# Performance work log

Hardware: AMD Instinct MI355X
Metric: run time of the kernel (lower is better)

The kernel has to match this reference:

```python
import jax, jax.numpy as jnp
import numpy as np

N, DIN, DOUT, E, K = 65536, 256, 256, 8, 2

def setup_inputs() -> dict:
    key = jax.random.key(0)
    k1, k2, k3, k4 = jax.random.split(key, 4)
    x = jax.random.normal(k1, (N, DIN), dtype=jnp.float32)
    Wr = jax.random.normal(k2, (DIN, E), dtype=jnp.float32) * (DIN ** -0.5)   # router Linear (no bias)
    We = jax.random.normal(k3, (E, DIN, DOUT), dtype=jnp.float32) * (DIN ** -0.5)  # expert Linear weights
    be = jax.random.normal(k4, (E, DOUT), dtype=jnp.float32) * 0.01               # expert Linear biases
    return {"x": x, "Wr": Wr, "We": We, "be": be}

def reference(x, Wr, We, be):
    # router: softmax over experts (eval mode -> no noise)
    probs = jax.nn.softmax(x @ Wr, axis=1)                    # [N, E]
    w, sel = jax.lax.top_k(probs, K)                          # [N, K]
    w = w / jnp.sum(w, axis=1, keepdims=True)                 # renormalize top-k weights
    # dense combine weights: scatter top-k weights back to [N, E]
    combine = jnp.zeros_like(probs).at[jnp.arange(x.shape[0])[:, None], sel].add(w)
    # all-expert outputs, then weighted combine (same math as gather/matmul/index_add loop)
    y_all = jnp.einsum('ni,eio->neo', x, We) + be[None, :, :]  # [N, E, DOUT]
    out = jnp.einsum('neo,ne->no', y_all, combine)             # [N, DOUT]
    return out
```

## Files before the change

kernel.cpp:

```cpp
#include <hip/hip_runtime.h>

#define N_TOK 65536
#define DIN   256
#define DOUT  256
#define NEXP  8
#define NPAIR 28

typedef __bf16 bf16x8 __attribute__((ext_vector_type(8)));
typedef __bf16 bf16x4 __attribute__((ext_vector_type(4)));
typedef float  f32x4  __attribute__((ext_vector_type(4)));

__device__ __forceinline__ void cp16_g2l(const void* g, void* l) {
  auto gp = (const __attribute__((address_space(1))) unsigned int*)(unsigned long long)g;
  auto lp = (__attribute__((address_space(3))) unsigned int*)(unsigned long long)l;
  __builtin_amdgcn_global_load_lds(gp, lp, 16, 0, 0);
}

__global__ __launch_bounds__(256) void prep_kernel(const float* __restrict__ We,
                                                   __bf16* __restrict__ Wt,
                                                   int* __restrict__ cnt) {
  __shared__ float T[64 * 65];
  int bid = blockIdx.x;
  if (bid == 0 && threadIdx.x < NPAIR) cnt[threadIdx.x] = 0;
  int e = bid >> 4;
  int tk = (bid >> 2) & 3, tn = bid & 3;
  int k0 = tk * 64, n0 = tn * 64;
  int tid = threadIdx.x;
  int cr = tid >> 6;
  int cc = tid & 63;
#pragma unroll
  for (int i = 0; i < 16; i++) {
    int k = i * 4 + cr;
    T[cc * 65 + k] = We[(size_t)(e * 256 + k0 + k) * 256 + n0 + cc];
  }
  __syncthreads();
#pragma unroll
  for (int i = 0; i < 16; i++) {
    int n = i * 4 + cr;
    Wt[(size_t)(e * 256 + n0 + n) * 256 + k0 + cc] = (__bf16)T[n * 65 + cc];
  }
}

__global__ __launch_bounds__(256) void router_kernel(const float* __restrict__ x,
                                                     const float* __restrict__ Wr,
                                                     __bf16* __restrict__ xb,
                                                     int* __restrict__ cnt,
                                                     unsigned short* __restrict__ pidx,
                                                     float* __restrict__ pw) {
  __shared__ float X[64 * 64];
  __shared__ float P[64 * 36];
  __shared__ int lcnt[NPAIR];
  __shared__ int gbase[NPAIR];
  int tid = threadIdx.x;
  if (tid < NPAIR) lcnt[tid] = 0;

  const int w = __builtin_amdgcn_readfirstlane(tid >> 6);
  const int t = tid & 63;
  int tokBase = blockIdx.x * 64;

  const int srow = tid >> 4;
  const int so16 = tid & 15;
  const int spo  = so16 ^ (srow & 7);

  float acc[NEXP];
#pragma unroll
  for (int e = 0; e < NEXP; e++) acc[e] = 0.f;

  float4 v[4];
#pragma unroll
  for (int i = 0; i < 4; i++)
    v[i] = *(const float4*)&x[(size_t)(tokBase + srow + 16 * i) * DIN + so16 * 4];

  for (int c = 0; c < 4; c++) {
#pragma unroll
    for (int i = 0; i < 4; i++) {
      int r = srow + 16 * i;
      *(float4*)&X[r * 64 + spo * 4] = v[i];
      bf16x4 bv;
      bv[0] = (__bf16)v[i].x; bv[1] = (__bf16)v[i].y;
      bv[2] = (__bf16)v[i].z; bv[3] = (__bf16)v[i].w;
      *(bf16x4*)&xb[(size_t)(tokBase + r) * DIN + c * 64 + so16 * 4] = bv;
    }
    __syncthreads();
    if (c < 3) {
#pragma unroll
      for (int i = 0; i < 4; i++)
        v[i] = *(const float4*)&x[(size_t)(tokBase + srow + 16 * i) * DIN + (c + 1) * 64 + so16 * 4];
    }
#pragma unroll
    for (int i4 = 0; i4 < 4; i4++) {
      int po = (w * 4 + i4) ^ (t & 7);
      float4 xv = *(const float4*)&X[t * 64 + po * 4];
      const float* w0 = &Wr[(c * 64 + w * 16 + i4 * 4) * NEXP];
#pragma unroll
      for (int e = 0; e < NEXP; e++)
        acc[e] += xv.x * w0[e] + xv.y * w0[NEXP + e] + xv.z * w0[2 * NEXP + e] + xv.w * w0[3 * NEXP + e];
    }
    __syncthreads();
  }

  f32x4 lo, hi;
#pragma unroll
  for (int e = 0; e < 4; e++) { lo[e] = acc[e]; hi[e] = acc[4 + e]; }
  *(f32x4*)&P[t * 36 + w * 8]     = lo;
  *(f32x4*)&P[t * 36 + w * 8 + 4] = hi;
  __syncthreads();
  if (tid >= 64) return;

  int token = tokBase + tid;

  f32x4 pa0 = *(const f32x4*)&P[tid * 36 + 0];
  f32x4 pa1 = *(const f32x4*)&P[tid * 36 + 8];
  f32x4 pa2 = *(const f32x4*)&P[tid * 36 + 16];
  f32x4 pa3 = *(const f32x4*)&P[tid * 36 + 24];
  f32x4 pb0 = *(const f32x4*)&P[tid * 36 + 4];
  f32x4 pb1 = *(const f32x4*)&P[tid * 36 + 12];
  f32x4 pb2 = *(const f32x4*)&P[tid * 36 + 20];
  f32x4 pb3 = *(const f32x4*)&P[tid * 36 + 28];
  f32x4 sA = ((pa0 + pa1) + pa2) + pa3;
  f32x4 sB = ((pb0 + pb1) + pb2) + pb3;
  float lg[NEXP];
#pragma unroll
  for (int e = 0; e < 4; e++) { lg[e] = sA[e]; lg[4 + e] = sB[e]; }

  int best = 0;
#pragma unroll
  for (int e = 1; e < NEXP; e++) if (lg[e] > lg[best]) best = e;
  int sec = (best == 0) ? 1 : 0;
#pragma unroll
  for (int e = 0; e < NEXP; e++)
    if (e != best && e != sec && lg[e] > lg[sec]) sec = e;
  float l3 = -1e30f;
#pragma unroll
  for (int e = 0; e < NEXP; e++)
    if (e != best && e != sec) l3 = fmaxf(l3, lg[e]);

  float diff = lg[sec] - lg[best];
  bool need = (lg[sec] - l3) < 5e-3f;
  if (__any(need)) {
    if (need) {
      const float4* xr = (const float4*)(x + (size_t)token * DIN);
      double d[NEXP];
#pragma unroll
      for (int e = 0; e < NEXP; e++) d[e] = 0.0;
      for (int i4 = 0; i4 < DIN / 4; i4++) {
        float4 vv = xr[i4];
        const float* w0 = &Wr[(i4 * 4) * NEXP];
#pragma unroll
        for (int e = 0; e < NEXP; e++)
          d[e] += (double)vv.x * w0[e] + (double)vv.y * w0[NEXP + e] +
                  (double)vv.z * w0[2 * NEXP + e] + (double)vv.w * w0[3 * NEXP + e];
      }
      best = 0;
#pragma unroll
      for (int e = 1; e < NEXP; e++) if (d[e] > d[best]) best = e;
      sec = (best == 0) ? 1 : 0;
#pragma unroll
      for (int e = 0; e < NEXP; e++)
        if (e != best && e != sec && d[e] > d[sec]) sec = e;
      diff = (float)(d[sec] - d[best]);
    }
  }

  float wb = 1.f / (1.f + expf(diff));
  int a, b2; float wa;
  if (best < sec) { a = best; b2 = sec; wa = wb; }
  else            { a = sec;  b2 = best; wa = 1.f - wb; }
  int p = a * (15 - a) / 2 + (b2 - a - 1);

  int lpos = atomicAdd(&lcnt[p], 1);
  if (tid < NPAIR) gbase[tid] = atomicAdd(&cnt[tid], lcnt[tid]);
  int pos = gbase[p] + lpos;
  pidx[p * N_TOK + pos] = (unsigned short)token;
  pw[p * N_TOK + pos] = wa;
}

__global__ __launch_bounds__(256, 2) void moe_gemm_kernel(const __bf16* __restrict__ xb,
                                                          const __bf16* __restrict__ Wt,
                                                          const float* __restrict__ be,
                                                          const int* __restrict__ cnt,
                                                          const unsigned short* __restrict__ pidx,
                                                          const float* __restrict__ pw,
                                                          float* __restrict__ out) {
  __shared__ __bf16 As[128 * 256];
  __shared__ unsigned short tokL[128];
  __shared__ float wL[128];
  __shared__ int meta[4];

  int tid = threadIdx.x;
  int bid = blockIdx.x;
  int nh = (bid >> 3) & 3;
  int tile = ((bid >> 5) << 3) | (bid & 7);

  if (tid == 0) {
    int s = 0, pp = -1, lt = 0, c = 0;
    for (int q = 0; q < NPAIR; q++) {
      int cq = cnt[q];
      int tq = (cq + 127) >> 7;
      if (tile < s + tq) { pp = q; lt = tile - s; c = cq; break; }
      s += tq;
    }
    meta[0] = pp; meta[1] = lt; meta[2] = c;
  }
  __syncthreads();
  int p = meta[0];
  if (p < 0) return;
  int lt = meta[1], cnt_p = meta[2];

  int a = 0, rem = p;
  while (rem >= 7 - a) { rem -= 7 - a; a++; }
  int b2 = a + 1 + rem;
  int r0 = lt * 128;

  if (tid < 128) {
    int gr = r0 + tid;
    tokL[tid] = (gr < cnt_p) ? pidx[p * N_TOK + gr] : (unsigned short)0;
    wL[tid]   = (gr < cnt_p) ? pw[p * N_TOK + gr] : 0.f;
  }
  __syncthreads();

  {
    const int r_base = tid >> 5;
    const int s8 = (tid & 31) ^ r_base;
#pragma unroll
    for (int i = 0; i < 16; i++) {
      int row = r_base + 8 * i;
      cp16_g2l(xb + (size_t)tokL[row] * DIN + s8 * 8, &As[(size_t)(tid + 256 * i) * 8]);
    }
  }
  __builtin_amdgcn_s_waitcnt(0x0F70);
  __syncthreads();

  const int lane = tid & 63, wid = tid >> 6;
  const int wm = wid & 1, wn = wid >> 1;
  const int c16 = lane & 15, quad = lane >> 4;

  const __bf16* WtA = Wt + ((size_t)a * DOUT + nh * 64) * DIN;
  const __bf16* WtB = Wt + ((size_t)b2 * DOUT + nh * 64) * DIN;

  f32x4 accA[4][2], accB[4][2];
#pragma unroll
  for (int mi = 0; mi < 4; mi++)
#pragma unroll
    for (int ni = 0; ni < 2; ni++)
#pragma unroll
      for (int r = 0; r < 4; r++) { accA[mi][ni][r] = 0.f; accB[mi][ni][r] = 0.f; }

#pragma unroll
  for (int kc = 0; kc < 4; kc++) {
#pragma unroll
    for (int ks = 0; ks < 2; ks++) {
      bf16x8 af[4], ba[2], bb[2];
      int oct = kc * 8 + ks * 4 + quad;
#pragma unroll
      for (int mi = 0; mi < 4; mi++) {
        int row = wm * 64 + mi * 16 + c16;
        af[mi] = *(const bf16x8*)&As[(size_t)(row * 32 + (oct ^ (row & 7))) * 8];
      }
#pragma unroll
      for (int ni = 0; ni < 2; ni++) {
        int col = wn * 32 + ni * 16 + c16;
        int koff = kc * 64 + ks * 32 + quad * 8;
        ba[ni] = *(const bf16x8*)&WtA[(size_t)col * DIN + koff];
        bb[ni] = *(const bf16x8*)&WtB[(size_t)col * DIN + koff];
      }
#pragma unroll
      for (int mi = 0; mi < 4; mi++)
#pragma unroll
        for (int ni = 0; ni < 2; ni++) {
          accA[mi][ni] = __builtin_amdgcn_mfma_f32_16x16x32_bf16(af[mi], ba[ni], accA[mi][ni], 0, 0, 0);
          accB[mi][ni] = __builtin_amdgcn_mfma_f32_16x16x32_bf16(af[mi], bb[ni], accB[mi][ni], 0, 0, 0);
        }
    }
  }

#pragma unroll
  for (int ni = 0; ni < 2; ni++) {
    int gcol = nh * 64 + wn * 32 + ni * 16 + c16;
    float bea = be[a * DOUT + gcol];
    float beb = be[b2 * DOUT + gcol];
#pragma unroll
    for (int mi = 0; mi < 4; mi++) {
#pragma unroll
      for (int r = 0; r < 4; r++) {
        int row = wm * 64 + mi * 16 + quad * 4 + r;
        if (r0 + row < cnt_p) {
          float w = wL[row];
          out[(size_t)tokL[row] * DOUT + gcol] =
              w * (accA[mi][ni][r] + bea) + (1.f - w) * (accB[mi][ni][r] + beb);
        }
      }
    }
  }
}

extern "C" void kernel_launch(void* const* d_in, const int* in_sizes, int n_in,
                              void* d_out, int out_size, void* d_ws, size_t ws_size,
                              hipStream_t stream) {
  const float* x  = (const float*)d_in[0];
  const float* Wr = (const float*)d_in[1];
  const float* We = (const float*)d_in[2];
  const float* be = (const float*)d_in[3];
  float* out = (float*)d_out;

  char* w = (char*)d_ws;
  __bf16* Wt = (__bf16*)w;
  __bf16* xb = (__bf16*)(w + (1u << 20));
  int* cnt = (int*)(w + (33u << 20));
  unsigned short* pidx = (unsigned short*)(w + (33u << 20) + 512);
  float* pw = (float*)(w + (33u << 20) + 512 + (size_t)NPAIR * N_TOK * 2);

  prep_kernel<<<128, 256, 0, stream>>>(We, Wt, cnt);
  router_kernel<<<N_TOK / 64, 256, 0, stream>>>(x, Wr, xb, cnt, pidx, pw);
  moe_gemm_kernel<<<2176, 256, 0, stream>>>(xb, Wt, be, cnt, pidx, pw, out);
}
```

Baseline: 218.6 us.

## Fuse router and dense all-expert GEMM into one per-token-block kernel

Replaces the router kernel (pair bucketing with atomics and scatter) and the gathered pair GEMM with one kernel. Each 64-token block converts x to bf16 in LDS, computes routing weights locally, then runs MFMA over all 8 experts with a weighted accumulate. This removes the bf16 activation round trip, the index/weight buffers, the atomics and a launch. In exchange it does 4x the matrix FLOPs, since the 6 experts with zero combine weight are still computed. The output is staged through LDS for coalesced stores.

```diff
diff --git a/kernel.cpp b/kernel.cpp
--- a/kernel.cpp
+++ b/kernel.cpp
@@ -4,24 +4,14 @@
 #define DIN   256
 #define DOUT  256
 #define NEXP  8
-#define NPAIR 28
 
 typedef __bf16 bf16x8 __attribute__((ext_vector_type(8)));
-typedef __bf16 bf16x4 __attribute__((ext_vector_type(4)));
 typedef float  f32x4  __attribute__((ext_vector_type(4)));
 
-__device__ __forceinline__ void cp16_g2l(const void* g, void* l) {
-  auto gp = (const __attribute__((address_space(1))) unsigned int*)(unsigned long long)g;
-  auto lp = (__attribute__((address_space(3))) unsigned int*)(unsigned long long)l;
-  __builtin_amdgcn_global_load_lds(gp, lp, 16, 0, 0);
-}
-
 __global__ __launch_bounds__(256) void prep_kernel(const float* __restrict__ We,
-                                                   __bf16* __restrict__ Wt,
-                                                   int* __restrict__ cnt) {
+                                                   __bf16* __restrict__ Wt) {
   __shared__ float T[64 * 65];
   int bid = blockIdx.x;
-  if (bid == 0 && threadIdx.x < NPAIR) cnt[threadIdx.x] = 0;
   int e = bid >> 4;
   int tk = (bid >> 2) & 3, tn = bid & 3;
   int k0 = tk * 64, n0 = tn * 64;
@@ -41,255 +31,198 @@
   }
 }
 
-__global__ __launch_bounds__(256) void router_kernel(const float* __restrict__ x,
-                                                     const float* __restrict__ Wr,
-                                                     __bf16* __restrict__ xb,
-                                                     int* __restrict__ cnt,
-                                                     unsigned short* __restrict__ pidx,
-                                                     float* __restrict__ pw) {
-  __shared__ float X[64 * 64];
+__global__ __launch_bounds__(256, 2) void moe_fused_kernel(const float* __restrict__ x,
+                                                           const float* __restrict__ Wr,
+                                                           const __bf16* __restrict__ Wt,
+                                                           const float* __restrict__ be,
+                                                           float* __restrict__ out) {
+  __shared__ __bf16 Xb[64 * 256];
   __shared__ float P[64 * 36];
-  __shared__ int lcnt[NPAIR];
-  __shared__ int gbase[NPAIR];
-  int tid = threadIdx.x;
-  if (tid < NPAIR) lcnt[tid] = 0;
+  __shared__ float C8[NEXP * 64];
+
+  const int tid = threadIdx.x;
+  const int tokBase = blockIdx.x * 64;
+
+  C8[tid] = 0.f;
+  C8[tid + 256] = 0.f;
+
+  {
+    const int srow = tid >> 5;
+    const int so   = tid & 31;
+    const int s8   = so ^ (srow & 7);
+#pragma unroll
+    for (int i = 0; i < 8; i++) {
+      int row = srow + 8 * i;
+      const float* src = &x[(size_t)(tokBase + row) * DIN + s8 * 8];
+      float4 u0 = *(const float4*)src;
+      float4 u1 = *(const float4*)(src + 4);
+      bf16x8 pk;
+      pk[0] = (__bf16)u0.x; pk[1] = (__bf16)u0.y; pk[2] = (__bf16)u0.z; pk[3] = (__bf16)u0.w;
+      pk[4] = (__bf16)u1.x; pk[5] = (__bf16)u1.y; pk[6] = (__bf16)u1.z; pk[7] = (__bf16)u1.w;
+      *(bf16x8*)&Xb[(row * 32 + so) * 8] = pk;
+    }
+  }
 
   const int w = __builtin_amdgcn_readfirstlane(tid >> 6);
   const int t = tid & 63;
-  int tokBase = blockIdx.x * 64;
-
-  const int srow = tid >> 4;
-  const int so16 = tid & 15;
-  const int spo  = so16 ^ (srow & 7);
-
-  float acc[NEXP];
-#pragma unroll
-  for (int e = 0; e < NEXP; e++) acc[e] = 0.f;
-
-  float4 v[4];
-#pragma unroll
-  for (int i = 0; i < 4; i++)
-    v[i] = *(const float4*)&x[(size_t)(tokBase + srow + 16 * i) * DIN + so16 * 4];
-
-  for (int c = 0; c < 4; c++) {
-#pragma unroll
-    for (int i = 0; i < 4; i++) {
-      int r = srow + 16 * i;
-      *(float4*)&X[r * 64 + spo * 4] = v[i];
-      bf16x4 bv;
-      bv[0] = (__bf16)v[i].x; bv[1] = (__bf16)v[i].y;
-      bv[2] = (__bf16)v[i].z; bv[3] = (__bf16)v[i].w;
-      *(bf16x4*)&xb[(size_t)(tokBase + r) * DIN + c * 64 + so16 * 4] = bv;
-    }
+  const int token = tokBase + t;
+  {
+    float a8[NEXP];
+#pragma unroll
+    for (int e = 0; e < NEXP; e++) a8[e] = 0.f;
+#pragma unroll
+    for (int i4 = 0; i4 < 16; i4++) {
+      int k = w * 64 + i4 * 4;
+      float4 xv = *(const float4*)&x[(size_t)token * DIN + k];
+      const float* w0 = &Wr[k * NEXP];
+#pragma unroll
+      for (int e = 0; e < NEXP; e++)
+        a8[e] += xv.x * w0[e] + xv.y * w0[NEXP + e] + xv.z * w0[2 * NEXP + e] + xv.w * w0[3 * NEXP + e];
+    }
+    f32x4 lo, hi;
+#pragma unroll
+    for (int e = 0; e < 4; e++) { lo[e] = a8[e]; hi[e] = a8[4 + e]; }
+    *(f32x4*)&P[t * 36 + w * 8]     = lo;
+    *(f32x4*)&P[t * 36 + w * 8 + 4] = hi;
+  }
+  __syncthreads();
+
+  if (tid < 64) {
+    f32x4 pa0 = *(const f32x4*)&P[tid * 36 + 0];
+    f32x4 pa1 = *(const f32x4*)&P[tid * 36 + 8];
+    f32x4 pa2 = *(const f32x4*)&P[tid * 36 + 16];
+    f32x4 pa3 = *(const f32x4*)&P[tid * 36 + 24];
+    f32x4 pb0 = *(const f32x4*)&P[tid * 36 + 4];
+    f32x4 pb1 = *(const f32x4*)&P[tid * 36 + 12];
+    f32x4 pb2 = *(const f32x4*)&P[tid * 36 + 20];
+    f32x4 pb3 = *(const f32x4*)&P[tid * 36 + 28];
+    f32x4 sA = ((pa0 + pa1) + pa2) + pa3;
+    f32x4 sB = ((pb0 + pb1) + pb2) + pb3;
+    float lg[NEXP];
+#pragma unroll
+    for (int e = 0; e < 4; e++) { lg[e] = sA[e]; lg[4 + e] = sB[e]; }
+
+    int best = 0;
+#pragma unroll
+    for (int e = 1; e < NEXP; e++) if (lg[e] > lg[best]) best = e;
+    int sec = (best == 0) ? 1 : 0;
+#pragma unroll
+    for (int e = 0; e < NEXP; e++)
+      if (e != best && e != sec && lg[e] > lg[sec]) sec = e;
+    float l3 = -1e30f;
+#pragma unroll
+    for (int e = 0; e < NEXP; e++)
+      if (e != best && e != sec) l3 = fmaxf(l3, lg[e]);
+
+    float diff = lg[sec] - lg[best];
+    bool need = (lg[sec] - l3) < 5e-3f;
+    if (__any(need)) {
+      if (need) {
+        const float4* xr = (const float4*)(x + (size_t)token * DIN);
+        double d[NEXP];
+#pragma unroll
+        for (int e = 0; e < NEXP; e++) d[e] = 0.0;
+        for (int i4 = 0; i4 < DIN / 4; i4++) {
+          float4 vv = xr[i4];
+          const float* w0 = &Wr[(i4 * 4) * NEXP];
+#pragma unroll
+          for (int e = 0; e < NEXP; e++)
+            d[e] += (double)vv.x * w0[e] + (double)vv.y * w0[NEXP + e] +
+                    (double)vv.z * w0[2 * NEXP + e] + (double)vv.w * w0[3 * NEXP + e];
+        }
+        best = 0;
+#pragma unroll
+        for (int e = 1; e < NEXP; e++) if (d[e] > d[best]) best = e;
+        sec = (best == 0) ? 1 : 0;
+#pragma unroll
+        for (int e = 0; e < NEXP; e++)
+          if (e != best && e != sec && d[e] > d[sec]) sec = e;
+        diff = (float)(d[sec] - d[best]);
+      }
+    }
+
+    float wb = 1.f / (1.f + expf(diff));
+    int a, b2; float wa;
+    if (best < sec) { a = best; b2 = sec; wa = wb; }
+    else            { a = sec;  b2 = best; wa = 1.f - wb; }
+    C8[a * 64 + tid]  = wa;
+    C8[b2 * 64 + tid] = 1.f - wa;
+  }
+  __syncthreads();
+
+  const int lane = tid & 63;
+  const int c16 = lane & 15, quad = lane >> 4;
+  const int wid = tid >> 6;
+
+  f32x4 oacc[4][4];
+#pragma unroll
+  for (int mi = 0; mi < 4; mi++)
+#pragma unroll
+    for (int ni = 0; ni < 4; ni++)
+#pragma unroll
+      for (int r = 0; r < 4; r++) oacc[mi][ni][r] = 0.f;
+
+  for (int e = 0; e < NEXP; e++) {
+    f32x4 t4[4][4];
+#pragma unroll
+    for (int mi = 0; mi < 4; mi++)
+#pragma unroll
+      for (int ni = 0; ni < 4; ni++)
+#pragma unroll
+        for (int r = 0; r < 4; r++) t4[mi][ni][r] = 0.f;
+
+#pragma unroll
+    for (int kk = 0; kk < 8; kk++) {
+      bf16x8 af[4];
+#pragma unroll
+      for (int mi = 0; mi < 4; mi++) {
+        int row = mi * 16 + c16;
+        int phys = (kk * 4 + quad) ^ (row & 7);
+        af[mi] = *(const bf16x8*)&Xb[(row * 32 + phys) * 8];
+      }
+#pragma unroll
+      for (int ni = 0; ni < 4; ni++) {
+        int col = wid * 64 + ni * 16 + c16;
+        bf16x8 bv = *(const bf16x8*)&Wt[((size_t)e * DOUT + col) * DIN + kk * 32 + quad * 8];
+#pragma unroll
+        for (int mi = 0; mi < 4; mi++)
+          t4[mi][ni] = __builtin_amdgcn_mfma_f32_16x16x32_bf16(af[mi], bv, t4[mi][ni], 0, 0, 0);
+      }
+    }
+#pragma unroll
+    for (int mi = 0; mi < 4; mi++) {
+      f32x4 wv = *(const f32x4*)&C8[e * 64 + mi * 16 + quad * 4];
+#pragma unroll
+      for (int ni = 0; ni < 4; ni++) {
+        float bias = be[e * DOUT + wid * 64 + ni * 16 + c16];
+        oacc[mi][ni] += wv * (t4[mi][ni] + bias);
+      }
+    }
+  }
+
+  float* OF = (float*)Xb;
+#pragma unroll
+  for (int h = 0; h < 2; h++) {
     __syncthreads();
-    if (c < 3) {
-#pragma unroll
-      for (int i = 0; i < 4; i++)
-        v[i] = *(const float4*)&x[(size_t)(tokBase + srow + 16 * i) * DIN + (c + 1) * 64 + so16 * 4];
-    }
-#pragma unroll
-    for (int i4 = 0; i4 < 4; i4++) {
-      int po = (w * 4 + i4) ^ (t & 7);
-      float4 xv = *(const float4*)&X[t * 64 + po * 4];
-      const float* w0 = &Wr[(c * 64 + w * 16 + i4 * 4) * NEXP];
-#pragma unroll
-      for (int e = 0; e < NEXP; e++)
-        acc[e] += xv.x * w0[e] + xv.y * w0[NEXP + e] + xv.z * w0[2 * NEXP + e] + xv.w * w0[3 * NEXP + e];
+    if ((wid >> 1) == h) {
+#pragma unroll
+      for (int mi = 0; mi < 4; mi++)
+#pragma unroll
+        for (int ni = 0; ni < 4; ni++)
+#pragma unroll
+          for (int r = 0; r < 4; r++) {
+            int row = mi * 16 + quad * 4 + r;
+            int colh = (wid & 1) * 64 + ni * 16 + c16;
+            OF[row * 128 + (colh ^ ((row & 7) << 2))] = oacc[mi][ni][r];
+          }
     }
     __syncthreads();
-  }
-
-  f32x4 lo, hi;
-#pragma unroll
-  for (int e = 0; e < 4; e++) { lo[e] = acc[e]; hi[e] = acc[4 + e]; }
-  *(f32x4*)&P[t * 36 + w * 8]     = lo;
-  *(f32x4*)&P[t * 36 + w * 8 + 4] = hi;
-  __syncthreads();
-  if (tid >= 64) return;
-
-  int token = tokBase + tid;
-
-  f32x4 pa0 = *(const f32x4*)&P[tid * 36 + 0];
-  f32x4 pa1 = *(const f32x4*)&P[tid * 36 + 8];
-  f32x4 pa2 = *(const f32x4*)&P[tid * 36 + 16];
-  f32x4 pa3 = *(const f32x4*)&P[tid * 36 + 24];
-  f32x4 pb0 = *(const f32x4*)&P[tid * 36 + 4];
-  f32x4 pb1 = *(const f32x4*)&P[tid * 36 + 12];
-  f32x4 pb2 = *(const f32x4*)&P[tid * 36 + 20];
-  f32x4 pb3 = *(const f32x4*)&P[tid * 36 + 28];
-  f32x4 sA = ((pa0 + pa1) + pa2) + pa3;
-  f32x4 sB = ((pb0 + pb1) + pb2) + pb3;
-  float lg[NEXP];
-#pragma unroll
-  for (int e = 0; e < 4; e++) { lg[e] = sA[e]; lg[4 + e] = sB[e]; }
-
-  int best = 0;
-#pragma unroll
-  for (int e = 1; e < NEXP; e++) if (lg[e] > lg[best]) best = e;
-  int sec = (best == 0) ? 1 : 0;
-#pragma unroll
-  for (int e = 0; e < NEXP; e++)
-    if (e != best && e != sec && lg[e] > lg[sec]) sec = e;
-  float l3 = -1e30f;
-#pragma unroll
-  for (int e = 0; e < NEXP; e++)
-    if (e != best && e != sec) l3 = fmaxf(l3, lg[e]);
-
-  float diff = lg[sec] - lg[best];
-  bool need = (lg[sec] - l3) < 5e-3f;
-  if (__any(need)) {
-    if (need) {
-      const float4* xr = (const float4*)(x + (size_t)token * DIN);
-      double d[NEXP];
-#pragma unroll
-      for (int e = 0; e < NEXP; e++) d[e] = 0.0;
-      for (int i4 = 0; i4 < DIN / 4; i4++) {
-        float4 vv = xr[i4];
-        const float* w0 = &Wr[(i4 * 4) * NEXP];
-#pragma unroll
-        for (int e = 0; e < NEXP; e++)
-          d[e] += (double)vv.x * w0[e] + (double)vv.y * w0[NEXP + e] +
-                  (double)vv.z * w0[2 * NEXP + e] + (double)vv.w * w0[3 * NEXP + e];
-      }
-      best = 0;
-#pragma unroll
-      for (int e = 1; e < NEXP; e++) if (d[e] > d[best]) best = e;
-      sec = (best == 0) ? 1 : 0;
-#pragma unroll
-      for (int e = 0; e < NEXP; e++)
-        if (e != best && e != sec && d[e] > d[sec]) sec = e;
-      diff = (float)(d[sec] - d[best]);
-    }
-  }
-
-  float wb = 1.f / (1.f + expf(diff));
-  int a, b2; float wa;
-  if (best < sec) { a = best; b2 = sec; wa = wb; }
-  else            { a = sec;  b2 = best; wa = 1.f - wb; }
-  int p = a * (15 - a) / 2 + (b2 - a - 1);
-
-  int lpos = atomicAdd(&lcnt[p], 1);
-  if (tid < NPAIR) gbase[tid] = atomicAdd(&cnt[tid], lcnt[tid]);
-  int pos = gbase[p] + lpos;
-  pidx[p * N_TOK + pos] = (unsigned short)token;
-  pw[p * N_TOK + pos] = wa;
-}
-
-__global__ __launch_bounds__(256, 2) void moe_gemm_kernel(const __bf16* __restrict__ xb,
-                                                          const __bf16* __restrict__ Wt,
-                                                          const float* __restrict__ be,
-                                                          const int* __restrict__ cnt,
-                                                          const unsigned short* __restrict__ pidx,
-                                                          const float* __restrict__ pw,
-                                                          float* __restrict__ out) {
-  __shared__ __bf16 As[128 * 256];
-  __shared__ unsigned short tokL[128];
-  __shared__ float wL[128];
-  __shared__ int meta[4];
-
-  int tid = threadIdx.x;
-  int bid = blockIdx.x;
-  int nh = (bid >> 3) & 3;
-  int tile = ((bid >> 5) << 3) | (bid & 7);
-
-  if (tid == 0) {
-    int s = 0, pp = -1, lt = 0, c = 0;
-    for (int q = 0; q < NPAIR; q++) {
-      int cq = cnt[q];
-      int tq = (cq + 127) >> 7;
-      if (tile < s + tq) { pp = q; lt = tile - s; c = cq; break; }
-      s += tq;
-    }
-    meta[0] = pp; meta[1] = lt; meta[2] = c;
-  }
-  __syncthreads();
-  int p = meta[0];
-  if (p < 0) return;
-  int lt = meta[1], cnt_p = meta[2];
-
-  int a = 0, rem = p;
-  while (rem >= 7 - a) { rem -= 7 - a; a++; }
-  int b2 = a + 1 + rem;
-  int r0 = lt * 128;
-
-  if (tid < 128) {
-    int gr = r0 + tid;
-    tokL[tid] = (gr < cnt_p) ? pidx[p * N_TOK + gr] : (unsigned short)0;
-    wL[tid]   = (gr < cnt_p) ? pw[p * N_TOK + gr] : 0.f;
-  }
-  __syncthreads();
-
-  {
-    const int r_base = tid >> 5;
-    const int s8 = (tid & 31) ^ r_base;
-#pragma unroll
-    for (int i = 0; i < 16; i++) {
-      int row = r_base + 8 * i;
-      cp16_g2l(xb + (size_t)tokL[row] * DIN + s8 * 8, &As[(size_t)(tid + 256 * i) * 8]);
-    }
-  }
-  __builtin_amdgcn_s_waitcnt(0x0F70);
-  __syncthreads();
-
-  const int lane = tid & 63, wid = tid >> 6;
-  const int wm = wid & 1, wn = wid >> 1;
-  const int c16 = lane & 15, quad = lane >> 4;
-
-  const __bf16* WtA = Wt + ((size_t)a * DOUT + nh * 64) * DIN;
-  const __bf16* WtB = Wt + ((size_t)b2 * DOUT + nh * 64) * DIN;
-
-  f32x4 accA[4][2], accB[4][2];
-#pragma unroll
-  for (int mi = 0; mi < 4; mi++)
-#pragma unroll
-    for (int ni = 0; ni < 2; ni++)
-#pragma unroll
-      for (int r = 0; r < 4; r++) { accA[mi][ni][r] = 0.f; accB[mi][ni][r] = 0.f; }
-
-#pragma unroll
-  for (int kc = 0; kc < 4; kc++) {
-#pragma unroll
-    for (int ks = 0; ks < 2; ks++) {
-      bf16x8 af[4], ba[2], bb[2];
-      int oct = kc * 8 + ks * 4 + quad;
-#pragma unroll
-      for (int mi = 0; mi < 4; mi++) {
-        int row = wm * 64 + mi * 16 + c16;
-        af[mi] = *(const bf16x8*)&As[(size_t)(row * 32 + (oct ^ (row & 7))) * 8];
-      }
-#pragma unroll
-      for (int ni = 0; ni < 2; ni++) {
-        int col = wn * 32 + ni * 16 + c16;
-        int koff = kc * 64 + ks * 32 + quad * 8;
-        ba[ni] = *(const bf16x8*)&WtA[(size_t)col * DIN + koff];
-        bb[ni] = *(const bf16x8*)&WtB[(size_t)col * DIN + koff];
-      }
-#pragma unroll
-      for (int mi = 0; mi < 4; mi++)
-#pragma unroll
-        for (int ni = 0; ni < 2; ni++) {
-          accA[mi][ni] = __builtin_amdgcn_mfma_f32_16x16x32_bf16(af[mi], ba[ni], accA[mi][ni], 0, 0, 0);
-          accB[mi][ni] = __builtin_amdgcn_mfma_f32_16x16x32_bf16(af[mi], bb[ni], accB[mi][ni], 0, 0, 0);
-        }
-    }
-  }
-
-#pragma unroll
-  for (int ni = 0; ni < 2; ni++) {
-    int gcol = nh * 64 + wn * 32 + ni * 16 + c16;
-    float bea = be[a * DOUT + gcol];
-    float beb = be[b2 * DOUT + gcol];
-#pragma unroll
-    for (int mi = 0; mi < 4; mi++) {
-#pragma unroll
-      for (int r = 0; r < 4; r++) {
-        int row = wm * 64 + mi * 16 + quad * 4 + r;
-        if (r0 + row < cnt_p) {
-          float w = wL[row];
-          out[(size_t)tokL[row] * DOUT + gcol] =
-              w * (accA[mi][ni][r] + bea) + (1.f - w) * (accB[mi][ni][r] + beb);
-        }
-      }
+#pragma unroll
+    for (int i = 0; i < 8; i++) {
+      int seg = tid + 256 * i;
+      int row = seg >> 5, cs = seg & 31;
+      f32x4 v = *(const f32x4*)&OF[row * 128 + ((cs * 4) ^ ((row & 7) << 2))];
+      *(f32x4*)&out[(size_t)(tokBase + row) * DOUT + h * 128 + cs * 4] = v;
     }
   }
 }
@@ -303,14 +236,8 @@
   const float* be = (const float*)d_in[3];
   float* out = (float*)d_out;
 
-  char* w = (char*)d_ws;
-  __bf16* Wt = (__bf16*)w;
-  __bf16* xb = (__bf16*)(w + (1u << 20));
-  int* cnt = (int*)(w + (33u << 20));
-  unsigned short* pidx = (unsigned short*)(w + (33u << 20) + 512);
-  float* pw = (float*)(w + (33u << 20) + 512 + (size_t)NPAIR * N_TOK * 2);
-
-  prep_kernel<<<128, 256, 0, stream>>>(We, Wt, cnt);
-  router_kernel<<<N_TOK / 64, 256, 0, stream>>>(x, Wr, xb, cnt, pidx, pw);
-  moe_gemm_kernel<<<2176, 256, 0, stream>>>(xb, Wt, be, cnt, pidx, pw, out);
+  __bf16* Wt = (__bf16*)d_ws;
+
+  prep_kernel<<<128, 256, 0, stream>>>(We, Wt);
+  moe_fused_kernel<<<N_TOK / 64, 256, 0, stream>>>(x, Wr, Wt, be, out);
 }
```

After: 400.0 us. +83.0%, slower.
